# Optimization experiments

Hardware: AMD Instinct MI355X
Metric: run time of the kernel (lower is better)

## Reference

```python
import jax, jax.numpy as jnp
import numpy as np

USER_NUM = 100000
ITEM_NUM = 50000
D = 64
E = 3200000
B = 16384


def setup_inputs() -> dict:
    key = jax.random.key(0)
    ks = jax.random.split(key, 12)
    user = jax.random.randint(ks[0], (B,), 0, USER_NUM)
    item_i = jax.random.randint(ks[1], (B,), 0, ITEM_NUM)
    item_j = jax.random.randint(ks[2], (B,), 0, ITEM_NUM)
    edge_u = jax.random.randint(ks[3], (E,), 0, USER_NUM)
    edge_i = jax.random.randint(ks[4], (E,), 0, ITEM_NUM)
    edge_val = jax.random.uniform(ks[5], (E,), dtype=jnp.float32)
    # nn.init.normal_(std=0.01)
    user_emb = 0.01 * jax.random.normal(ks[6], (USER_NUM, D), dtype=jnp.float32)
    item_emb = 0.01 * jax.random.normal(ks[7], (ITEM_NUM, D), dtype=jnp.float32)
    old_U_emb = 0.01 * jax.random.normal(ks[8], (USER_NUM, D), dtype=jnp.float32)
    old_I_emb = 0.01 * jax.random.normal(ks[9], (ITEM_NUM, D), dtype=jnp.float32)
    n_U = jax.random.uniform(ks[10], (USER_NUM,), dtype=jnp.float32)
    n_U = n_U / jnp.linalg.norm(n_U)  # pre_self normalizes by L2 norm
    n_I = jax.random.uniform(ks[11], (ITEM_NUM,), dtype=jnp.float32)
    n_I = n_I / jnp.linalg.norm(n_I)
    return {"user": user, "item_i": item_i, "item_j": item_j,
            "edge_u": edge_u, "edge_i": edge_i, "edge_val": edge_val,
            "user_emb": user_emb, "item_emb": item_emb,
            "old_U_emb": old_U_emb, "old_I_emb": old_I_emb,
            "n_U": n_U, "n_I": n_I}


def _spmm(seg_ids, gather_ids, vals, x, num_segments):
    # one hop of sparse adjacency @ dense embeddings: gather -> scale -> scatter-add
    msg = vals[:, None] * x[gather_ids]          # [E, D]
    return jax.ops.segment_sum(msg, seg_ids, num_segments=num_segments)


def reference(user, item_i, item_j, edge_u, edge_i, edge_val,
              user_emb, item_emb, old_U_emb, old_I_emb, n_U, n_I):
    # 3-hop LightGCN-style propagation over bipartite graph
    g1u = _spmm(edge_u, edge_i, edge_val, item_emb, USER_NUM)
    g1i = _spmm(edge_i, edge_u, edge_val, user_emb, ITEM_NUM)
    g2u = _spmm(edge_u, edge_i, edge_val, g1i, USER_NUM)
    g2i = _spmm(edge_i, edge_u, edge_val, g1u, ITEM_NUM)
    g3u = _spmm(edge_u, edge_i, edge_val, g2i, USER_NUM)
    g3i = _spmm(edge_i, edge_u, edge_val, g2u, ITEM_NUM)
    gcn_u = user_emb + 0.5 * g1u + (1.0 / 3.0) * g2u + 0.25 * g3u
    gcn_i = item_emb + 0.5 * g1i + (1.0 / 3.0) * g2i + 0.25 * g3i

    # BPR loss
    u = gcn_u[user]
    ii = gcn_i[item_i]
    ij = gcn_i[item_j]
    pred_i = jnp.sum(u * ii, axis=-1)
    pred_j = jnp.sum(u * ij, axis=-1)
    bpr = -jnp.mean(jax.nn.log_sigmoid(pred_i - pred_j))
    reg = 1e-4 * jnp.mean(jnp.sum(u ** 2 + ii ** 2 + ij ** 2, axis=-1))
    loss_bpr = bpr + reg

    # self-distillation loss (loss_self)
    Ud = jnp.linalg.norm(old_U_emb - gcn_u, axis=1)  # [USER_NUM]
    Id = jnp.linalg.norm(old_I_emb - gcn_i, axis=1)  # [ITEM_NUM]
    loss_self = jnp.dot(Ud, n_U) / USER_NUM + jnp.dot(Id, n_I) / ITEM_NUM

    return jnp.stack([loss_bpr, 100.0 * loss_self,
                      jnp.float32(1.0), jnp.float32(1.0)])
```

## Files before the change

kernel.cpp:

```cpp
#include <hip/hip_runtime.h>

#define USER_NUM 100000
#define ITEM_NUM 50000
#define DD 64
#define NEDGE 3200000
#define NB 16384
#define NSLOT 256

#define ATILE 8192
#define NTILE ((NEDGE + ATILE - 1) / ATILE)
#define USH 9
#define ISH 8
#define UBK ((USER_NUM + (1 << USH) - 1) >> USH)
#define IBK ((ITEM_NUM + (1 << ISH) - 1) >> ISH)
#define NBK (UBK + IBK)
#define CPAD 16
#define HIST_GRID 784

#define FP8_SCALE 64.0f

typedef float v2f __attribute__((ext_vector_type(2)));

__device__ __forceinline__ float waveReduceSum(float x) {
#pragma unroll
    for (int off = 32; off > 0; off >>= 1)
        x += __shfl_down(x, off, 64);
    return x;
}

__device__ __forceinline__ unsigned roundbf(unsigned y) {
    return (y + 0x7fffu + ((y >> 16) & 1u)) >> 16;
}

__device__ __forceinline__ void dec8(const uint2 b, float* f) {
    v2f f0 = __builtin_amdgcn_cvt_pk_f32_fp8(b.x, false);
    v2f f1 = __builtin_amdgcn_cvt_pk_f32_fp8(b.x, true);
    v2f f2 = __builtin_amdgcn_cvt_pk_f32_fp8(b.y, false);
    v2f f3 = __builtin_amdgcn_cvt_pk_f32_fp8(b.y, true);
    f[0] = f0.x; f[1] = f0.y; f[2] = f1.x; f[3] = f1.y;
    f[4] = f2.x; f[5] = f2.y; f[6] = f3.x; f[7] = f3.y;
}
__device__ __forceinline__ void fma8p(const uint2 b, const float v, v2f* a) {
    v2f f0 = __builtin_amdgcn_cvt_pk_f32_fp8(b.x, false);
    v2f f1 = __builtin_amdgcn_cvt_pk_f32_fp8(b.x, true);
    v2f f2 = __builtin_amdgcn_cvt_pk_f32_fp8(b.y, false);
    v2f f3 = __builtin_amdgcn_cvt_pk_f32_fp8(b.y, true);
    const v2f vv = {v, v};
    a[0] += vv * f0;
    a[1] += vv * f1;
    a[2] += vv * f2;
    a[3] += vv * f3;
}
__device__ __forceinline__ uint2 pack_fp8x8(const float* a) {
    int lo = 0, hi = 0;
    lo = __builtin_amdgcn_cvt_pk_fp8_f32(a[0], a[1], lo, false);
    lo = __builtin_amdgcn_cvt_pk_fp8_f32(a[2], a[3], lo, true);
    hi = __builtin_amdgcn_cvt_pk_fp8_f32(a[4], a[5], hi, false);
    hi = __builtin_amdgcn_cvt_pk_fp8_f32(a[6], a[7], hi, true);
    return make_uint2((unsigned)lo, (unsigned)hi);
}

__global__ void __launch_bounds__(256) cvt8_kernel(
    const float4* __restrict__ src, uint2* __restrict__ dst, int n8) {
    int t = blockIdx.x * blockDim.x + threadIdx.x;
    if (t < n8) {
        float4 a = src[2 * t], b = src[2 * t + 1];
        float f[8] = {a.x * FP8_SCALE, a.y * FP8_SCALE, a.z * FP8_SCALE, a.w * FP8_SCALE,
                      b.x * FP8_SCALE, b.y * FP8_SCALE, b.z * FP8_SCALE, b.w * FP8_SCALE};
        dst[t] = pack_fp8x8(f);
    }
}


__global__ void __launch_bounds__(256) coarse_hist(
    const int4* __restrict__ eu4, const int4* __restrict__ ei4,
    int* __restrict__ coarseCnt) {
    __shared__ int lc[NBK];
    const int t = threadIdx.x;
    for (int j = t; j < NBK; j += 256) lc[j] = 0;
    __syncthreads();
    for (int k = blockIdx.x * 256 + t; k < NEDGE / 4; k += HIST_GRID * 256) {
        int4 u = eu4[k];
        int4 i = ei4[k];
        atomicAdd(&lc[u.x >> USH], 1); atomicAdd(&lc[u.y >> USH], 1);
        atomicAdd(&lc[u.z >> USH], 1); atomicAdd(&lc[u.w >> USH], 1);
        atomicAdd(&lc[UBK + (i.x >> ISH)], 1); atomicAdd(&lc[UBK + (i.y >> ISH)], 1);
        atomicAdd(&lc[UBK + (i.z >> ISH)], 1); atomicAdd(&lc[UBK + (i.w >> ISH)], 1);
    }
    __syncthreads();
    for (int j = t; j < NBK; j += 256)
        if (lc[j]) atomicAdd(&coarseCnt[j * CPAD], lc[j]);
}

__global__ void __launch_bounds__(512) coarse_scan(
    const int* __restrict__ cnt, int* __restrict__ base, int* __restrict__ cur) {
    __shared__ int a[512];
    const int t = threadIdx.x;
    int v = (t < UBK) ? cnt[t * CPAD] : 0;
    a[t] = v;
    __syncthreads();
    for (int off = 1; off < 512; off <<= 1) {
        int x = (t >= off) ? a[t - off] : 0;
        __syncthreads();
        a[t] += x;
        __syncthreads();
    }
    if (t < UBK) { base[t] = a[t] - v; cur[t * CPAD] = a[t] - v; }
    __syncthreads();
    v = (t < IBK) ? cnt[(UBK + t) * CPAD] : 0;
    a[t] = v;
    __syncthreads();
    for (int off = 1; off < 512; off <<= 1) {
        int x = (t >= off) ? a[t - off] : 0;
        __syncthreads();
        a[t] += x;
        __syncthreads();
    }
    if (t < IBK) { base[UBK + t] = a[t] - v; cur[(UBK + t) * CPAD] = a[t] - v; }
}

__global__ void __launch_bounds__(256, 2) binA(
    const int* __restrict__ eu, const int* __restrict__ ei,
    const float* __restrict__ ev,
    int* __restrict__ ccur,
    int2* __restrict__ stU, int2* __restrict__ stI) {
    __shared__ int2 pay[ATILE];
    __shared__ unsigned char sbid[ATILE];
    __shared__ int hist[256];
    __shared__ int pscan[256];
    __shared__ int cursor[256];
    __shared__ int delta[256];

    const int t = threadIdx.x;
    const int dirI = blockIdx.y;
    const int tb = blockIdx.x * ATILE;
    const int n = min(ATILE, NEDGE - tb);
    const int* key = dirI ? ei : eu;
    const int SH = dirI ? ISH : USH;

    hist[t] = 0;
    __syncthreads();
    for (int k = t; k < n; k += 256)
        atomicAdd(&hist[key[tb + k] >> SH], 1);
    __syncthreads();
    pscan[t] = hist[t];
    __syncthreads();
    for (int off = 1; off < 256; off <<= 1) {
        int x = (t >= off) ? pscan[t - off] : 0;
        __syncthreads();
        pscan[t] += x;
        __syncthreads();
    }
    {
        const int c = hist[t];
        const int lst = pscan[t] - c;
        cursor[t] = lst;
        int gp = 0;
        if (c > 0) {
            int* gc = dirI ? (ccur + UBK * CPAD) : ccur;
            gp = atomicAdd(&gc[t * CPAD], c);
        }
        delta[t] = gp - lst;
    }
    __syncthreads();
    if (dirI == 0) {
        for (int k = t; k < n; k += 256) {
            const int e = tb + k;
            const int u = eu[e], i = ei[e];
            const int b = u >> USH;
            const int p = atomicAdd(&cursor[b], 1);
            pay[p] = make_int2(((u & ((1 << USH) - 1)) << 16) | i,
                               __float_as_int(ev[e]));
            sbid[p] = (unsigned char)b;
        }
    } else {
        for (int k = t; k < n; k += 256) {
            const int e = tb + k;
            const int u = eu[e], i = ei[e];
            const int b = i >> ISH;
            const int p = atomicAdd(&cursor[b], 1);
            pay[p] = make_int2(((i & ((1 << ISH) - 1)) << 17) | u,
                               __float_as_int(ev[e]));
            sbid[p] = (unsigned char)b;
        }
    }
    __syncthreads();
    int2* st = dirI ? stI : stU;
    for (int p = t; p < n; p += 256)
        st[delta[sbid[p]] + p] = pay[p];
}

__global__ void __launch_bounds__(256) binB(
    const int2* __restrict__ stU, const int2* __restrict__ stI,
    const int* __restrict__ base, const int* __restrict__ cnt,
    int* __restrict__ rpU, int* __restrict__ rpI,
    unsigned* __restrict__ ivU, unsigned* __restrict__ ivI) {
    __shared__ int h[512];
    const int t = threadIdx.x;
    const int b = blockIdx.x;
    if (b < UBK) {
        const int s = base[b], n = cnt[b * CPAD];
        const int dbase = b << USH;
        h[t] = 0; h[t + 256] = 0;
        __syncthreads();
        for (int p = s + t; p < s + n; p += 256)
            atomicAdd(&h[(unsigned)stU[p].x >> 16], 1);
        __syncthreads();
        int o0 = h[t], o1 = h[t + 256];
        for (int off = 1; off < 512; off <<= 1) {
            int x0 = (t >= off) ? h[t - off] : 0;
            int x1 = (t + 256 >= off) ? h[t + 256 - off] : 0;
            __syncthreads();
            h[t] += x0; h[t + 256] += x1;
            __syncthreads();
        }
        int e0 = s + h[t] - o0, e1 = s + h[t + 256] - o1;
        __syncthreads();
        h[t] = e0; h[t + 256] = e1;
        if (dbase + t < USER_NUM) rpU[dbase + t] = e0;
        if (dbase + 256 + t < USER_NUM) rpU[dbase + 256 + t] = e1;
        if (t == 0 && dbase + 512 >= USER_NUM) rpU[USER_NUM] = s + n;
        __syncthreads();
        for (int p = s + t; p < s + n; p += 256) {
            int2 en = stU[p];
            unsigned x = (unsigned)en.x;
            int pos = atomicAdd(&h[x >> 16], 1);
            unsigned bf = roundbf((unsigned)en.y);
            ivU[pos] = (bf << 16) | (x & 0xFFFFu);
        }
    } else {
        const int ib = b - UBK;
        const int s = base[b], n = cnt[b * CPAD];
        const int dbase = ib << ISH;
        h[t] = 0;
        __syncthreads();
        for (int p = s + t; p < s + n; p += 256)
            atomicAdd(&h[(unsigned)stI[p].x >> 17], 1);
        __syncthreads();
        int o0 = h[t];
        for (int off = 1; off < 256; off <<= 1) {
            int x0 = (t >= off) ? h[t - off] : 0;
            __syncthreads();
            h[t] += x0;
            __syncthreads();
        }
        int e0 = s + h[t] - o0;
        __syncthreads();
        h[t] = e0;
        if (dbase + t < ITEM_NUM) rpI[dbase + t] = e0;
        if (t == 0 && dbase + 256 >= ITEM_NUM) rpI[ITEM_NUM] = s + n;
        __syncthreads();
        for (int p = s + t; p < s + n; p += 256) {
            int2 en = stI[p];
            unsigned x = (unsigned)en.x;
            int pos = atomicAdd(&h[x >> 17], 1);
            unsigned v15 = roundbf((unsigned)en.y) & 0x7FFFu;
            ivI[pos] = (v15 << 17) | (x & 0x1FFFFu);
        }
    }
}

#define UW (USER_NUM / 8)
#define IW (ITEM_NUM / 8)

template<bool ISU>
__device__ __forceinline__ void row_accum_own(
    const int* __restrict__ rp, const unsigned* __restrict__ iv,
    const uint2* __restrict__ src, int row, int r, float* acc) {
    const int s = rp[row], e2 = rp[row + 1];
    v2f a0[4] = {{0.f, 0.f}, {0.f, 0.f}, {0.f, 0.f}, {0.f, 0.f}};
    v2f a1[4] = {{0.f, 0.f}, {0.f, 0.f}, {0.f, 0.f}, {0.f, 0.f}};
    int t = s;
    for (; t + 3 < e2; t += 4) {
        const unsigned q0 = iv[t];
        const unsigned q1 = iv[t + 1];
        const unsigned q2 = iv[t + 2];
        const unsigned q3 = iv[t + 3];
        const float v0 = ISU ? __uint_as_float(q0 & 0xFFFF0000u)
                             : __uint_as_float((q0 >> 17) << 16);
        const float v1 = ISU ? __uint_as_float(q1 & 0xFFFF0000u)
                             : __uint_as_float((q1 >> 17) << 16);
        const float v2 = ISU ? __uint_as_float(q2 & 0xFFFF0000u)
                             : __uint_as_float((q2 >> 17) << 16);
        const float v3 = ISU ? __uint_as_float(q3 & 0xFFFF0000u)
                             : __uint_as_float((q3 >> 17) << 16);
        const int x0 = ISU ? (int)(q0 & 0xFFFFu) : (int)(q0 & 0x1FFFFu);
        const int x1 = ISU ? (int)(q1 & 0xFFFFu) : (int)(q1 & 0x1FFFFu);
        const int x2 = ISU ? (int)(q2 & 0xFFFFu) : (int)(q2 & 0x1FFFFu);
        const int x3 = ISU ? (int)(q3 & 0xFFFFu) : (int)(q3 & 0x1FFFFu);
        const uint2 b0 = src[x0 * 8 + r];
        const uint2 b1 = src[x1 * 8 + r];
        const uint2 b2 = src[x2 * 8 + r];
        const uint2 b3 = src[x3 * 8 + r];
        fma8p(b0, v0, a0);
        fma8p(b1, v1, a1);
        fma8p(b2, v2, a0);
        fma8p(b3, v3, a1);
    }
    for (; t < e2; ++t) {
        const unsigned q0 = iv[t];
        const float v0 = ISU ? __uint_as_float(q0 & 0xFFFF0000u)
                             : __uint_as_float((q0 >> 17) << 16);
        const int x0 = ISU ? (int)(q0 & 0xFFFFu) : (int)(q0 & 0x1FFFFu);
        fma8p(src[x0 * 8 + r], v0, a0);
    }
#pragma unroll
    for (int k = 0; k < 4; k++) {
        const v2f sv = a0[k] + a1[k];
        acc[2 * k]     = sv.x;
        acc[2 * k + 1] = sv.y;
    }
}

__global__ void __launch_bounds__(256) gather_hop_f8(
    const int* __restrict__ rpU, const unsigned* __restrict__ ivU,
    const uint2* __restrict__ srcForU, uint2* __restrict__ outU,
    const int* __restrict__ rpI, const unsigned* __restrict__ ivI,
    const uint2* __restrict__ srcForI, uint2* __restrict__ outI) {
    const int lane = threadIdx.x & 63;
    const int sub = lane >> 3;
    const int r = lane & 7;
    const int wave = blockIdx.x * 4 + (threadIdx.x >> 6);
    float acc[8];
    if (wave < UW) {
        const int row = wave * 8 + sub;
        row_accum_own<true>(rpU, ivU, srcForU, row, r, acc);
        outU[row * 8 + r] = pack_fp8x8(acc);
    } else if (wave < UW + IW) {
        const int row = (wave - UW) * 8 + sub;
        row_accum_own<false>(rpI, ivI, srcForI, row, r, acc);
        outI[row * 8 + r] = pack_fp8x8(acc);
    }
}

__global__ void __launch_bounds__(256) gather_hop3(
    const int* __restrict__ rpU, const unsigned* __restrict__ ivU,
    const uint2* __restrict__ srcForU,
    const int* __restrict__ rpI, const unsigned* __restrict__ ivI,
    const uint2* __restrict__ srcForI,
    const float4* __restrict__ embU, const uint2* __restrict__ g1u,
    const uint2* __restrict__ g2u, float4* __restrict__ gcnU,
    const float4* __restrict__ embI, const uint2* __restrict__ g1i,
    const uint2* __restrict__ g2i, float4* __restrict__ gcnI) {
    const int lane = threadIdx.x & 63;
    const int sub = lane >> 3;
    const int r = lane & 7;
    const int wave = blockIdx.x * 4 + (threadIdx.x >> 6);
    float acc[8];
    const float4* emb; const uint2* g1; const uint2* g2; float4* gcn; int row;
    if (wave < UW) {
        row = wave * 8 + sub;
        row_accum_own<true>(rpU, ivU, srcForU, row, r, acc);
        emb = embU; g1 = g1u; g2 = g2u; gcn = gcnU;
    } else if (wave < UW + IW) {
        row = (wave - UW) * 8 + sub;
        row_accum_own<false>(rpI, ivI, srcForI, row, r, acc);
        emb = embI; g1 = g1i; g2 = g2i; gcn = gcnI;
    } else return;
    {
        const float C1 = 0.5f / FP8_SCALE;
        const float C2 = (1.0f / 3.0f) / FP8_SCALE;
        const float C3 = 0.25f / FP8_SCALE;
        float f1[8], f2[8];
        dec8(g1[row * 8 + r], f1);
        dec8(g2[row * 8 + r], f2);
        const float4 e0 = emb[row * 16 + 2 * r];
        const float4 e1 = emb[row * 16 + 2 * r + 1];
        float4 o0, o1;
        o0.x = e0.x + C1 * f1[0] + C2 * f2[0] + C3 * acc[0];
        o0.y = e0.y + C1 * f1[1] + C2 * f2[1] + C3 * acc[1];
        o0.z = e0.z + C1 * f1[2] + C2 * f2[2] + C3 * acc[2];
        o0.w = e0.w + C1 * f1[3] + C2 * f2[3] + C3 * acc[3];
        o1.x = e1.x + C1 * f1[4] + C2 * f2[4] + C3 * acc[4];
        o1.y = e1.y + C1 * f1[5] + C2 * f2[5] + C3 * acc[5];
        o1.z = e1.z + C1 * f1[6] + C2 * f2[6] + C3 * acc[6];
        o1.w = e1.w + C1 * f1[7] + C2 * f2[7] + C3 * acc[7];
        gcn[row * 16 + 2 * r] = o0;
        gcn[row * 16 + 2 * r + 1] = o1;
    }
}

__global__ void __launch_bounds__(256) bpr_loss(
    const int* __restrict__ user, const int* __restrict__ itemI,
    const int* __restrict__ itemJ,
    const float4* __restrict__ gcnU4, const float4* __restrict__ gcnI4,
    float* __restrict__ accs) {
    const int lane = threadIdx.x & 63;
    const int sub = lane >> 4;
    const int r = lane & 15;
    const int W = blockIdx.x * 4 + (threadIdx.x >> 6);
    const int NW = gridDim.x * 4;
    float accB = 0.0f, accR = 0.0f;
    for (int g = W; g < NB / 4; g += NW) {
        const int samp = g * 4 + sub;
        const int uu = user[samp], vi = itemI[samp], vj = itemJ[samp];
        const float4 u  = gcnU4[uu * 16 + r];
        const float4 xi = gcnI4[vi * 16 + r];
        const float4 xj = gcnI4[vj * 16 + r];
        float pi = u.x * xi.x + u.y * xi.y + u.z * xi.z + u.w * xi.w;
        float pj = u.x * xj.x + u.y * xj.y + u.z * xj.z + u.w * xj.w;
        float rg = u.x * u.x + u.y * u.y + u.z * u.z + u.w * u.w
                 + xi.x * xi.x + xi.y * xi.y + xi.z * xi.z + xi.w * xi.w
                 + xj.x * xj.x + xj.y * xj.y + xj.z * xj.z + xj.w * xj.w;
#pragma unroll
        for (int off = 1; off <= 8; off <<= 1) {
            pi += __shfl_xor(pi, off, 64);
            pj += __shfl_xor(pj, off, 64);
            rg += __shfl_xor(rg, off, 64);
        }
        if (r == 0) {
            const float x = pi - pj;
            accB += fmaxf(-x, 0.0f) + log1pf(expf(-fabsf(x)));
            accR += rg;
        }
    }
    accB = waveReduceSum(accB);
    accR = waveReduceSum(accR);
    if (lane == 0) {
        const int slot = W & (NSLOT - 1);
        unsafeAtomicAdd(&accs[0 * NSLOT + slot], accB);
        unsafeAtomicAdd(&accs[1 * NSLOT + slot], accR);
    }
}

__global__ void __launch_bounds__(256) self_loss(
    const float4* __restrict__ oldU4, const float4* __restrict__ oldI4,
    const float4* __restrict__ gcnU4, const float4* __restrict__ gcnI4,
    const float* __restrict__ nU, const float* __restrict__ nI,
    float* __restrict__ accs) {
    const int lane = threadIdx.x & 63;
    const int sub = lane >> 4;
    const int r = lane & 15;
    const int W = blockIdx.x * 4 + (threadIdx.x >> 6);
    const int NW = gridDim.x * 4;
    const int ngroups = (USER_NUM + ITEM_NUM) / 4;
    float accU = 0.0f, accI = 0.0f;
    for (int g = W; g < ngroups; g += NW) {
        const int row = g * 4 + sub;
        const bool isU = row < USER_NUM;
        const int rr = isU ? row : row - USER_NUM;
        const float4 o  = isU ? oldU4[rr * 16 + r] : oldI4[rr * 16 + r];
        const float4 gg = isU ? gcnU4[rr * 16 + r] : gcnI4[rr * 16 + r];
        const float dx = o.x - gg.x, dy = o.y - gg.y;
        const float dz = o.z - gg.z, dw = o.w - gg.w;
        float s = dx * dx + dy * dy + dz * dz + dw * dw;
#pragma unroll
        for (int off = 1; off <= 8; off <<= 1)
            s += __shfl_xor(s, off, 64);
        if (r == 0) {
            const float val = sqrtf(s) * (isU ? nU[rr] : nI[rr]);
            if (isU) accU += val; else accI += val;
        }
    }
    accU = waveReduceSum(accU);
    accI = waveReduceSum(accI);
    if (lane == 0) {
        const int slot = W & (NSLOT - 1);
        unsafeAtomicAdd(&accs[2 * NSLOT + slot], accU);
        unsafeAtomicAdd(&accs[3 * NSLOT + slot], accI);
    }
}

__global__ void __launch_bounds__(64) finalize(const float* __restrict__ accs,
                                               float* __restrict__ out) {
    const int lane = threadIdx.x;
    float s[4];
#pragma unroll
    for (int k = 0; k < 4; k++) {
        float v = 0.0f;
        for (int j = lane; j < NSLOT; j += 64) v += accs[k * NSLOT + j];
        s[k] = waveReduceSum(v);
    }
    if (lane == 0) {
        const float loss_bpr = s[0] / NB + 1e-4f * (s[1] / NB);
        const float loss_self = s[2] / USER_NUM + s[3] / ITEM_NUM;
        out[0] = loss_bpr;
        out[1] = 100.0f * loss_self;
        out[2] = 1.0f;
        out[3] = 1.0f;
    }
}

extern "C" void kernel_launch(void* const* d_in, const int* in_sizes, int n_in,
                              void* d_out, int out_size, void* d_ws, size_t ws_size,
                              hipStream_t stream) {
    const int*   user     = (const int*)d_in[0];
    const int*   item_i   = (const int*)d_in[1];
    const int*   item_j   = (const int*)d_in[2];
    const int*   edge_u   = (const int*)d_in[3];
    const int*   edge_i   = (const int*)d_in[4];
    const float* edge_val = (const float*)d_in[5];
    const float* user_emb = (const float*)d_in[6];
    const float* item_emb = (const float*)d_in[7];
    const float* old_U    = (const float*)d_in[8];
    const float* old_I    = (const float*)d_in[9];
    const float* n_U      = (const float*)d_in[10];
    const float* n_I      = (const float*)d_in[11];
    float* out = (float*)d_out;

    char* base = (char*)d_ws;
    size_t off = 0;
    auto carve = [&](size_t bytes) {
        char* p = base + off;
        off += (bytes + 255) & ~(size_t)255;
        return p;
    };
    int*      coarseCnt = (int*)carve(NBK * CPAD * 4);
    float*    accs      = (float*)carve(4 * NSLOT * 4);
    size_t zero_bytes = off;
    int*      cbase = (int*)carve(NBK * 4);
    int*      ccur  = (int*)carve(NBK * CPAD * 4);
    int*      rpU   = (int*)carve((USER_NUM + 1) * 4);
    int*      rpI   = (int*)carve((ITEM_NUM + 1) * 4);
    unsigned* ivU   = (unsigned*)carve((size_t)NEDGE * 4);
    unsigned* ivI   = (unsigned*)carve((size_t)NEDGE * 4);
    uint2*    ebU8  = (uint2*)carve((size_t)USER_NUM * DD);
    uint2*    ebI8  = (uint2*)carve((size_t)ITEM_NUM * DD);
    uint2*    g1u8  = (uint2*)carve((size_t)USER_NUM * DD);
    uint2*    g1i8  = (uint2*)carve((size_t)ITEM_NUM * DD);
    uint2*    g2u8  = (uint2*)carve((size_t)USER_NUM * DD);
    uint2*    g2i8  = (uint2*)carve((size_t)ITEM_NUM * DD);
    int2*     stU   = (int2*)carve((size_t)NEDGE * 8);
    int2*     stI   = (int2*)carve((size_t)NEDGE * 8);
    float* gcnU = (float*)stU;
    float* gcnI = (float*)stI;

    hipMemsetAsync(d_ws, 0, zero_bytes, stream);

    const dim3 blk(256);

    cvt8_kernel<<<(USER_NUM * 8 + 255) / 256, blk, 0, stream>>>(
        (const float4*)user_emb, ebU8, USER_NUM * 8);
    cvt8_kernel<<<(ITEM_NUM * 8 + 255) / 256, blk, 0, stream>>>(
        (const float4*)item_emb, ebI8, ITEM_NUM * 8);

    coarse_hist<<<HIST_GRID, blk, 0, stream>>>((const int4*)edge_u,
                                               (const int4*)edge_i, coarseCnt);
    coarse_scan<<<1, 512, 0, stream>>>(coarseCnt, cbase, ccur);
    binA<<<dim3(NTILE, 2), blk, 0, stream>>>(edge_u, edge_i, edge_val,
                                             ccur, stU, stI);
    binB<<<NBK, blk, 0, stream>>>(stU, stI, cbase, coarseCnt, rpU, rpI, ivU, ivI);

    const int hop_waves = UW + IW;
    const int hop_grid = (hop_waves + 3) / 4;

    gather_hop_f8<<<hop_grid, blk, 0, stream>>>(rpU, ivU, ebI8, g1u8,
                                                rpI, ivI, ebU8, g1i8);
    gather_hop_f8<<<hop_grid, blk, 0, stream>>>(rpU, ivU, g1i8, g2u8,
                                                rpI, ivI, g1u8, g2i8);
    gather_hop3<<<hop_grid, blk, 0, stream>>>(
        rpU, ivU, g2i8, rpI, ivI, g2u8,
        (const float4*)user_emb, g1u8, g2u8, (float4*)gcnU,
        (const float4*)item_emb, g1i8, g2i8, (float4*)gcnI);

    bpr_loss<<<128, blk, 0, stream>>>(user, item_i, item_j,
                                      (const float4*)gcnU, (const float4*)gcnI, accs);
    self_loss<<<256, blk, 0, stream>>>(
        (const float4*)old_U, (const float4*)old_I,
        (const float4*)gcnU, (const float4*)gcnI, n_U, n_I, accs);
    finalize<<<1, 64, 0, stream>>>(accs, out);
}
```

Before: 593.3 us.

## Pad CSR rows to multiples of four for vectorized edge loads in gather

```diff
diff --git a/kernel.cpp b/kernel.cpp
--- a/kernel.cpp
+++ b/kernel.cpp
@@ -7,7 +7,7 @@
 #define NB 16384
 #define NSLOT 256
 
-#define ATILE 8192
+#define ATILE 4096
 #define NTILE ((NEDGE + ATILE - 1) / ATILE)
 #define USH 9
 #define ISH 8
@@ -119,7 +119,7 @@
     if (t < IBK) { base[UBK + t] = a[t] - v; cur[(UBK + t) * CPAD] = a[t] - v; }
 }
 
-__global__ void __launch_bounds__(256, 2) binA(
+__global__ void __launch_bounds__(256, 4) binA(
     const int* __restrict__ eu, const int* __restrict__ ei,
     const float* __restrict__ ev,
     int* __restrict__ ccur,
@@ -201,12 +201,17 @@
     if (b < UBK) {
         const int s = base[b], n = cnt[b * CPAD];
         const int dbase = b << USH;
+        const int s_al = s + 4 * dbase;
         h[t] = 0; h[t + 256] = 0;
         __syncthreads();
         for (int p = s + t; p < s + n; p += 256)
             atomicAdd(&h[(unsigned)stU[p].x >> 16], 1);
         __syncthreads();
-        int o0 = h[t], o1 = h[t + 256];
+        const int o0 = h[t], o1 = h[t + 256];
+        const int a0c = (o0 + 3) & ~3, a1c = (o1 + 3) & ~3;
+        __syncthreads();
+        h[t] = a0c; h[t + 256] = a1c;
+        __syncthreads();
         for (int off = 1; off < 512; off <<= 1) {
             int x0 = (t >= off) ? h[t - off] : 0;
             int x1 = (t + 256 >= off) ? h[t + 256 - off] : 0;
@@ -214,12 +219,20 @@
             h[t] += x0; h[t + 256] += x1;
             __syncthreads();
         }
-        int e0 = s + h[t] - o0, e1 = s + h[t + 256] - o1;
+        const int e0 = s_al + h[t] - a0c;
+        const int e1 = s_al + h[t + 256] - a1c;
+        const int alignedTotal = h[511];
         __syncthreads();
         h[t] = e0; h[t + 256] = e1;
         if (dbase + t < USER_NUM) rpU[dbase + t] = e0;
         if (dbase + 256 + t < USER_NUM) rpU[dbase + 256 + t] = e1;
-        if (t == 0 && dbase + 512 >= USER_NUM) rpU[USER_NUM] = s + n;
+        if (t == 0 && dbase + 512 >= USER_NUM) rpU[USER_NUM] = s_al + alignedTotal;
+        for (int k = o0; k < a0c; k++) ivU[e0 + k] = 0u;
+        for (int k = o1; k < a1c; k++) ivU[e1 + k] = 0u;
+        if (dbase + 512 < USER_NUM) {
+            const int gapEnd = (s + n) + 4 * (dbase + 512);
+            for (int p = s_al + alignedTotal + t; p < gapEnd; p += 256) ivU[p] = 0u;
+        }
         __syncthreads();
         for (int p = s + t; p < s + n; p += 256) {
             int2 en = stU[p];
@@ -232,23 +245,34 @@
         const int ib = b - UBK;
         const int s = base[b], n = cnt[b * CPAD];
         const int dbase = ib << ISH;
+        const int s_al = s + 4 * dbase;
         h[t] = 0;
         __syncthreads();
         for (int p = s + t; p < s + n; p += 256)
             atomicAdd(&h[(unsigned)stI[p].x >> 17], 1);
         __syncthreads();
-        int o0 = h[t];
+        const int o0 = h[t];
+        const int a0c = (o0 + 3) & ~3;
+        __syncthreads();
+        h[t] = a0c;
+        __syncthreads();
         for (int off = 1; off < 256; off <<= 1) {
             int x0 = (t >= off) ? h[t - off] : 0;
             __syncthreads();
             h[t] += x0;
             __syncthreads();
         }
-        int e0 = s + h[t] - o0;
+        const int e0 = s_al + h[t] - a0c;
+        const int alignedTotal = h[255];
         __syncthreads();
         h[t] = e0;
         if (dbase + t < ITEM_NUM) rpI[dbase + t] = e0;
-        if (t == 0 && dbase + 256 >= ITEM_NUM) rpI[ITEM_NUM] = s + n;
+        if (t == 0 && dbase + 256 >= ITEM_NUM) rpI[ITEM_NUM] = s_al + alignedTotal;
+        for (int k = o0; k < a0c; k++) ivI[e0 + k] = 0u;
+        if (dbase + 256 < ITEM_NUM) {
+            const int gapEnd = (s + n) + 4 * (dbase + 256);
+            for (int p = s_al + alignedTotal + t; p < gapEnd; p += 256) ivI[p] = 0u;
+        }
         __syncthreads();
         for (int p = s + t; p < s + n; p += 256) {
             int2 en = stI[p];
@@ -268,42 +292,46 @@
     const int* __restrict__ rp, const unsigned* __restrict__ iv,
     const uint2* __restrict__ src, int row, int r, float* acc) {
     const int s = rp[row], e2 = rp[row + 1];
+    const uint2* __restrict__ srcr = src + r;
     v2f a0[4] = {{0.f, 0.f}, {0.f, 0.f}, {0.f, 0.f}, {0.f, 0.f}};
     v2f a1[4] = {{0.f, 0.f}, {0.f, 0.f}, {0.f, 0.f}, {0.f, 0.f}};
     int t = s;
-    for (; t + 3 < e2; t += 4) {
-        const unsigned q0 = iv[t];
-        const unsigned q1 = iv[t + 1];
-        const unsigned q2 = iv[t + 2];
-        const unsigned q3 = iv[t + 3];
-        const float v0 = ISU ? __uint_as_float(q0 & 0xFFFF0000u)
-                             : __uint_as_float((q0 >> 17) << 16);
-        const float v1 = ISU ? __uint_as_float(q1 & 0xFFFF0000u)
-                             : __uint_as_float((q1 >> 17) << 16);
-        const float v2 = ISU ? __uint_as_float(q2 & 0xFFFF0000u)
-                             : __uint_as_float((q2 >> 17) << 16);
-        const float v3 = ISU ? __uint_as_float(q3 & 0xFFFF0000u)
-                             : __uint_as_float((q3 >> 17) << 16);
-        const int x0 = ISU ? (int)(q0 & 0xFFFFu) : (int)(q0 & 0x1FFFFu);
-        const int x1 = ISU ? (int)(q1 & 0xFFFFu) : (int)(q1 & 0x1FFFFu);
-        const int x2 = ISU ? (int)(q2 & 0xFFFFu) : (int)(q2 & 0x1FFFFu);
-        const int x3 = ISU ? (int)(q3 & 0xFFFFu) : (int)(q3 & 0x1FFFFu);
-        const uint2 b0 = src[x0 * 8 + r];
-        const uint2 b1 = src[x1 * 8 + r];
-        const uint2 b2 = src[x2 * 8 + r];
-        const uint2 b3 = src[x3 * 8 + r];
-        fma8p(b0, v0, a0);
-        fma8p(b1, v1, a1);
-        fma8p(b2, v2, a0);
-        fma8p(b3, v3, a1);
-    }
-    for (; t < e2; ++t) {
-        const unsigned q0 = iv[t];
-        const float v0 = ISU ? __uint_as_float(q0 & 0xFFFF0000u)
-                             : __uint_as_float((q0 >> 17) << 16);
-        const int x0 = ISU ? (int)(q0 & 0xFFFFu) : (int)(q0 & 0x1FFFFu);
-        fma8p(src[x0 * 8 + r], v0, a0);
-    }
+#define XOF(q) (ISU ? (int)((q) & 0xFFFFu) : (int)((q) & 0x1FFFFu))
+#define VOF(q) (ISU ? __uint_as_float((q) & 0xFFFF0000u) \
+                    : __uint_as_float(((q) >> 17) << 16))
+    for (; t + 8 <= e2; t += 8) {
+        const uint4 qa = *(const uint4*)(iv + t);
+        const uint4 qb = *(const uint4*)(iv + t + 4);
+        const uint2 b0 = srcr[XOF(qa.x) * 8];
+        const uint2 b1 = srcr[XOF(qa.y) * 8];
+        const uint2 b2 = srcr[XOF(qa.z) * 8];
+        const uint2 b3 = srcr[XOF(qa.w) * 8];
+        const uint2 b4 = srcr[XOF(qb.x) * 8];
+        const uint2 b5 = srcr[XOF(qb.y) * 8];
+        const uint2 b6 = srcr[XOF(qb.z) * 8];
+        const uint2 b7 = srcr[XOF(qb.w) * 8];
+        fma8p(b0, VOF(qa.x), a0);
+        fma8p(b1, VOF(qa.y), a1);
+        fma8p(b2, VOF(qa.z), a0);
+        fma8p(b3, VOF(qa.w), a1);
+        fma8p(b4, VOF(qb.x), a0);
+        fma8p(b5, VOF(qb.y), a1);
+        fma8p(b6, VOF(qb.z), a0);
+        fma8p(b7, VOF(qb.w), a1);
+    }
+    if (t < e2) {
+        const uint4 qa = *(const uint4*)(iv + t);
+        const uint2 b0 = srcr[XOF(qa.x) * 8];
+        const uint2 b1 = srcr[XOF(qa.y) * 8];
+        const uint2 b2 = srcr[XOF(qa.z) * 8];
+        const uint2 b3 = srcr[XOF(qa.w) * 8];
+        fma8p(b0, VOF(qa.x), a0);
+        fma8p(b1, VOF(qa.y), a1);
+        fma8p(b2, VOF(qa.z), a0);
+        fma8p(b3, VOF(qa.w), a1);
+    }
+#undef XOF
+#undef VOF
 #pragma unroll
     for (int k = 0; k < 4; k++) {
         const v2f sv = a0[k] + a1[k];
@@ -512,8 +540,8 @@
     int*      ccur  = (int*)carve(NBK * CPAD * 4);
     int*      rpU   = (int*)carve((USER_NUM + 1) * 4);
     int*      rpI   = (int*)carve((ITEM_NUM + 1) * 4);
-    unsigned* ivU   = (unsigned*)carve((size_t)NEDGE * 4);
-    unsigned* ivI   = (unsigned*)carve((size_t)NEDGE * 4);
+    unsigned* ivU   = (unsigned*)carve(((size_t)NEDGE + 4 * USER_NUM + 2048) * 4);
+    unsigned* ivI   = (unsigned*)carve(((size_t)NEDGE + 4 * ITEM_NUM + 2048) * 4);
     uint2*    ebU8  = (uint2*)carve((size_t)USER_NUM * DD);
     uint2*    ebI8  = (uint2*)carve((size_t)ITEM_NUM * DD);
     uint2*    g1u8  = (uint2*)carve((size_t)USER_NUM * DD);
```

Result: slower. 1.047 ms (+76.5%).
